# Optimization experiments

Measured on AMD Instinct MI355X. Metric: run time of the kernel, lower is better.

The kernel has to match this reference:

```python
import jax, jax.numpy as jnp
import numpy as np

MARGIN = 0.3
EPS = 1e-12


def setup_inputs() -> dict:
    key = jax.random.key(0)
    k1, k2 = jax.random.split(key)
    n, d = 4096, 1024
    inputs = jax.random.normal(k1, (n, d), dtype=jnp.float32)
    targets = jax.random.randint(k2, (n,), 0, 64, dtype=jnp.int64)
    return {"inputs": inputs, "targets": targets}


def reference(inputs, targets):
    n = inputs.shape[0]
    # pairwise Euclidean distance matrix: ||xi||^2 + ||xj||^2 - 2 xi.xj
    sq = jnp.sum(inputs * inputs, axis=1)  # [n]
    dist2 = sq[:, None] + sq[None, :] - 2.0 * (inputs @ inputs.T)
    dist = jnp.sqrt(jnp.clip(dist2, EPS))  # [n, n]
    # same-label mask (includes diagonal, matching original)
    mask = targets[:, None] == targets[None, :]
    # fused masked row-wise hard mining
    neg_inf = jnp.asarray(-jnp.inf, dist.dtype)
    pos_inf = jnp.asarray(jnp.inf, dist.dtype)
    dist_ap = jnp.max(jnp.where(mask, dist, neg_inf), axis=1)  # hardest positive
    dist_an = jnp.min(jnp.where(mask, pos_inf, dist), axis=1)  # hardest negative
    # MarginRankingLoss with y=1: mean(relu(margin - (dist_an - dist_ap)))
    loss = jnp.mean(jnp.maximum(MARGIN - (dist_an - dist_ap), 0.0))
    prec = jnp.sum((dist_an > dist_ap).astype(jnp.float32)) / n
    return (loss, prec)
```

## Files before the change

### kernel.cpp

```cpp
#include <hip/hip_runtime.h>
#include <stdint.h>

#define MARGIN 0.3f
#define EPS 1e-12f

typedef __attribute__((ext_vector_type(8))) __bf16 bf16x8;
typedef __attribute__((ext_vector_type(4))) float f32x4;

__device__ __forceinline__ unsigned short f2bf(float f) {
    unsigned u = __float_as_uint(f);
    unsigned r = (u + 0x7FFFu + ((u >> 16) & 1u)) >> 16;
    return (unsigned short)r;
}

#define GLD16(gp, lp)                                                     \
    __builtin_amdgcn_global_load_lds(                                     \
        (const __attribute__((address_space(1))) void*)(gp),              \
        (__attribute__((address_space(3))) void*)(lp), 16, 0, 0)

__global__ __launch_bounds__(256) void prep_kernel(
    const float* __restrict__ X, unsigned short* __restrict__ Xbf,
    float* __restrict__ sqg, unsigned* __restrict__ apb,
    unsigned* __restrict__ anb, unsigned* __restrict__ ctr, int d) {
    const int row = blockIdx.x;
    const int tid = threadIdx.x;
    const float4* Xr = (const float4*)(X + (size_t)row * d);
    float s = 0.0f;
    for (int idx = tid; idx < (d >> 2); idx += blockDim.x) {
        float4 v = Xr[idx];
        s += v.x * v.x + v.y * v.y + v.z * v.z + v.w * v.w;
        ushort4 o;
        o.x = f2bf(v.x); o.y = f2bf(v.y); o.z = f2bf(v.z); o.w = f2bf(v.w);
        ((ushort4*)(Xbf + (size_t)row * d))[idx] = o;
    }
    __shared__ float red[4];
    for (int off = 32; off > 0; off >>= 1) s += __shfl_down(s, off, 64);
    const int wave = tid >> 6, lane = tid & 63;
    if (lane == 0) red[wave] = s;
    __syncthreads();
    if (tid == 0) {
        sqg[row] = red[0] + red[1] + red[2] + red[3];
        apb[row] = 0u;
        anb[row] = 0x7F800000u;
        if (row == 0) ctr[0] = 0u;
    }
}

#define BM 128
#define BN 128
#define BK 32

__global__ __launch_bounds__(256) void tri_gemm(
    const unsigned short* __restrict__ Xbf, const float* __restrict__ sqg,
    const int* __restrict__ tgt, unsigned* __restrict__ apb,
    unsigned* __restrict__ anb, unsigned* __restrict__ ctr,
    float* __restrict__ out, int n, int d, int nblk) {
    __shared__ unsigned short ldsA[2][BM * BK];
    __shared__ unsigned short ldsB[2][BN * BK];

    const int tid  = threadIdx.x;
    const int lane = tid & 63;
    const int wave = tid >> 6;
    const int wm = wave >> 1, wn = wave & 1;
    const int lo = lane & 15, hi = lane >> 4;

    const int bid = blockIdx.x;
    int bi = (int)((sqrtf(8.0f * (float)bid + 1.0f) - 1.0f) * 0.5f);
    while ((bi + 1) * (bi + 2) / 2 <= bid) ++bi;
    while (bi * (bi + 1) / 2 > bid) --bi;
    const int bj = bid - bi * (bi + 1) / 2;
    const int rowBase = bi * BM;
    const int colBase = bj * BN;
    const bool offdiag = (bi != bj);

    const int lrow = lane >> 2;
    const int lk   = (lane & 3) * 8;

    f32x4 acc[4][4] = {};

    const int nt = d / BK;
    int cur = 0;
#pragma unroll
    for (int c2 = 0; c2 < 2; ++c2) {
        const int c = wave * 2 + c2;
        GLD16(Xbf + (size_t)(rowBase + c * 16 + lrow) * d + lk, &ldsA[0][c * 512]);
        GLD16(Xbf + (size_t)(colBase + c * 16 + lrow) * d + lk, &ldsB[0][c * 512]);
    }
    asm volatile("s_waitcnt vmcnt(0)" ::: "memory");
    __syncthreads();

    for (int t = 0; t < nt; ++t) {
        if (t + 1 < nt) {
            const int k0 = (t + 1) * BK;
#pragma unroll
            for (int c2 = 0; c2 < 2; ++c2) {
                const int c = wave * 2 + c2;
                GLD16(Xbf + (size_t)(rowBase + c * 16 + lrow) * d + k0 + lk,
                      &ldsA[cur ^ 1][c * 512]);
                GLD16(Xbf + (size_t)(colBase + c * 16 + lrow) * d + k0 + lk,
                      &ldsB[cur ^ 1][c * 512]);
            }
        }
        bf16x8 a[4], b[4];
#pragma unroll
        for (int mi = 0; mi < 4; ++mi)
            a[mi] = *(const bf16x8*)&ldsA[cur][(wm * 64 + mi * 16 + lo) * BK + hi * 8];
#pragma unroll
        for (int ni = 0; ni < 4; ++ni)
            b[ni] = *(const bf16x8*)&ldsB[cur][(wn * 64 + ni * 16 + lo) * BK + hi * 8];
#pragma unroll
        for (int mi = 0; mi < 4; ++mi)
#pragma unroll
            for (int ni = 0; ni < 4; ++ni)
                acc[mi][ni] = __builtin_amdgcn_mfma_f32_16x16x32_bf16(
                    a[mi], b[ni], acc[mi][ni], 0, 0, 0);
        if (t + 1 < nt) {
            asm volatile("s_waitcnt vmcnt(0)" ::: "memory");
            __syncthreads();
            cur ^= 1;
        }
    }

    float sqj[4];
    int   tj[4];
#pragma unroll
    for (int ni = 0; ni < 4; ++ni) {
        const int gj = colBase + wn * 64 + ni * 16 + lo;
        sqj[ni] = sqg[gj];
        tj[ni]  = tgt[gj];
    }
    float cap[4], can[4];
#pragma unroll
    for (int ni = 0; ni < 4; ++ni) { cap[ni] = 0.0f; can[ni] = __uint_as_float(0x7F800000u); }

#pragma unroll
    for (int mi = 0; mi < 4; ++mi) {
#pragma unroll
        for (int j = 0; j < 4; ++j) {
            const int gi = rowBase + wm * 64 + mi * 16 + hi * 4 + j;
            const float sqi = sqg[gi];
            const int   ti  = tgt[gi];
            float ap = 0.0f;
            float an = __uint_as_float(0x7F800000u);
#pragma unroll
            for (int ni = 0; ni < 4; ++ni) {
                const float d2 = sqi + sqj[ni] - 2.0f * acc[mi][ni][j];
                const float dist = sqrtf(fmaxf(d2, EPS));
                if (ti == tj[ni]) {
                    ap = fmaxf(ap, dist);
                    cap[ni] = fmaxf(cap[ni], dist);
                } else {
                    an = fminf(an, dist);
                    can[ni] = fminf(can[ni], dist);
                }
            }
#pragma unroll
            for (int m = 1; m < 16; m <<= 1) {
                ap = fmaxf(ap, __shfl_xor(ap, m, 64));
                an = fminf(an, __shfl_xor(an, m, 64));
            }
            if (lo == 0) {
                atomicMax(&apb[gi], __float_as_uint(ap));
                atomicMin(&anb[gi], __float_as_uint(an));
            }
        }
    }
    if (offdiag) {
#pragma unroll
        for (int ni = 0; ni < 4; ++ni) {
            float ap = cap[ni], an = can[ni];
#pragma unroll
            for (int m = 16; m < 64; m <<= 1) {
                ap = fmaxf(ap, __shfl_xor(ap, m, 64));
                an = fminf(an, __shfl_xor(an, m, 64));
            }
            if (hi == 0) {
                const int gj = colBase + wn * 64 + ni * 16 + lo;
                atomicMax(&apb[gj], __float_as_uint(ap));
                atomicMin(&anb[gj], __float_as_uint(an));
            }
        }
    }

    __threadfence();
    __syncthreads();
    __shared__ int lastFlag;
    if (tid == 0) {
        unsigned prev = __hip_atomic_fetch_add(ctr, 1u, __ATOMIC_ACQ_REL,
                                               __HIP_MEMORY_SCOPE_AGENT);
        lastFlag = (prev == (unsigned)(nblk - 1)) ? 1 : 0;
    }
    __syncthreads();
    if (lastFlag) {
        float ls = 0.0f, pc = 0.0f;
        for (int i = tid; i < n; i += 256) {
            const float ap = __uint_as_float(__hip_atomic_load(
                &apb[i], __ATOMIC_RELAXED, __HIP_MEMORY_SCOPE_AGENT));
            const float an = __uint_as_float(__hip_atomic_load(
                &anb[i], __ATOMIC_RELAXED, __HIP_MEMORY_SCOPE_AGENT));
            ls += fmaxf(MARGIN - (an - ap), 0.0f);
            pc += (an > ap) ? 1.0f : 0.0f;
        }
        __shared__ float rl[4], rp[4];
        for (int off = 32; off > 0; off >>= 1) {
            ls += __shfl_down(ls, off, 64);
            pc += __shfl_down(pc, off, 64);
        }
        if ((tid & 63) == 0) { rl[tid >> 6] = ls; rp[tid >> 6] = pc; }
        __syncthreads();
        if (tid == 0) {
            out[0] = (rl[0] + rl[1] + rl[2] + rl[3]) / (float)n;
            out[1] = (rp[0] + rp[1] + rp[2] + rp[3]) / (float)n;
        }
    }
}

__global__ __launch_bounds__(256) void fb_zero(float* __restrict__ out) {
    if (threadIdx.x == 0) { out[0] = 0.0f; out[1] = 0.0f; }
}

__global__ __launch_bounds__(256) void fb_row(
    const float* __restrict__ X, const int* __restrict__ tgt,
    float* __restrict__ out, int n, int d) {
    __shared__ float xi[4096];
    const int i = blockIdx.x;
    const int tid = threadIdx.x;
    for (int k = tid; k < d; k += 256) xi[k] = X[(size_t)i * d + k];
    __syncthreads();
    const int ti = tgt[i];
    float ap = 0.0f;
    float an = __uint_as_float(0x7F800000u);
    for (int j = tid; j < n; j += 256) {
        const float4* Xj = (const float4*)(X + (size_t)j * d);
        float s = 0.0f;
        for (int k4 = 0; k4 < (d >> 2); ++k4) {
            float4 v = Xj[k4];
            float4 u = *(const float4*)&xi[k4 * 4];
            float dx = u.x - v.x, dy = u.y - v.y, dz = u.z - v.z, dw = u.w - v.w;
            s += dx * dx + dy * dy + dz * dz + dw * dw;
        }
        const float dist = sqrtf(fmaxf(s, EPS));
        if (tgt[j] == ti) ap = fmaxf(ap, dist);
        else              an = fminf(an, dist);
    }
    for (int m = 1; m < 64; m <<= 1) {
        ap = fmaxf(ap, __shfl_xor(ap, m, 64));
        an = fminf(an, __shfl_xor(an, m, 64));
    }
    __shared__ float rap[4], ran[4];
    const int wave = tid >> 6, lane = tid & 63;
    if (lane == 0) { rap[wave] = ap; ran[wave] = an; }
    __syncthreads();
    if (tid == 0) {
        ap = fmaxf(fmaxf(rap[0], rap[1]), fmaxf(rap[2], rap[3]));
        an = fminf(fminf(ran[0], ran[1]), fminf(ran[2], ran[3]));
        atomicAdd(&out[0], fmaxf(MARGIN - (an - ap), 0.0f));
        atomicAdd(&out[1], (an > ap) ? 1.0f : 0.0f);
    }
}

__global__ __launch_bounds__(64) void fb_scale(float* __restrict__ out, float inv_n) {
    if (threadIdx.x == 0) { out[0] *= inv_n; out[1] *= inv_n; }
}

extern "C" void kernel_launch(void* const* d_in, const int* in_sizes, int n_in,
                              void* d_out, int out_size, void* d_ws, size_t ws_size,
                              hipStream_t stream) {
    const float* X   = (const float*)d_in[0];
    const int*   tgt = (const int*)d_in[1];
    const int n = in_sizes[1];
    const int d = in_sizes[0] / n;

    const size_t need = (size_t)n * d * 2 + (size_t)n * 4 * 3 + 4;
    if (ws_size >= need) {
        char* ws = (char*)d_ws;
        unsigned short* Xbf = (unsigned short*)ws;
        float*    sqg = (float*)(ws + (size_t)n * d * 2);
        unsigned* apb = (unsigned*)((char*)sqg + (size_t)n * 4);
        unsigned* anb = apb + n;
        unsigned* ctr = anb + n;

        const int nb = n / BM;
        const int nblk = nb * (nb + 1) / 2;
        prep_kernel<<<n, 256, 0, stream>>>(X, Xbf, sqg, apb, anb, ctr, d);
        tri_gemm<<<nblk, 256, 0, stream>>>(Xbf, sqg, tgt, apb, anb, ctr,
                                           (float*)d_out, n, d, nblk);
    } else {
        fb_zero<<<1, 256, 0, stream>>>((float*)d_out);
        fb_row<<<n, 256, 0, stream>>>(X, tgt, (float*)d_out, n, d);
        fb_scale<<<1, 64, 0, stream>>>((float*)d_out, 1.0f / (float)n);
    }
}
```

Baseline: 146.3 us.

## Load GEMM operands directly from global to registers, remap blocks per XCD

The triangular GEMM drops the LDS double-buffered global_load_lds staging. Each wave now loads its bf16 fragments straight from global memory into registers, ping-ponging two register sets across K steps with no barriers. Block IDs are remapped so consecutive tiles land on the same XCD for L2 locality, and the prep kernel now gives each wave one row. The cost is that tiles are no longer shared through LDS, so each wave re-reads from L2/global and global traffic grows, with uncoalesced 16-byte row-strided accesses.

After: 223.8 us. 1.53x slower.

```diff
diff --git a/kernel.cpp b/kernel.cpp
--- a/kernel.cpp
+++ b/kernel.cpp
@@ -13,37 +13,30 @@
     return (unsigned short)r;
 }
 
-#define GLD16(gp, lp)                                                     \
-    __builtin_amdgcn_global_load_lds(                                     \
-        (const __attribute__((address_space(1))) void*)(gp),              \
-        (__attribute__((address_space(3))) void*)(lp), 16, 0, 0)
-
 __global__ __launch_bounds__(256) void prep_kernel(
     const float* __restrict__ X, unsigned short* __restrict__ Xbf,
     float* __restrict__ sqg, unsigned* __restrict__ apb,
     unsigned* __restrict__ anb, unsigned* __restrict__ ctr, int d) {
-    const int row = blockIdx.x;
-    const int tid = threadIdx.x;
+    const int wave = threadIdx.x >> 6, lane = threadIdx.x & 63;
+    const int row = blockIdx.x * 4 + wave;
     const float4* Xr = (const float4*)(X + (size_t)row * d);
+    ushort4* Or = (ushort4*)(Xbf + (size_t)row * d);
     float s = 0.0f;
-    for (int idx = tid; idx < (d >> 2); idx += blockDim.x) {
-        float4 v = Xr[idx];
+    const int nq = d >> 2;
+    for (int i = lane; i < nq; i += 64) {
+        float4 v = Xr[i];
         s += v.x * v.x + v.y * v.y + v.z * v.z + v.w * v.w;
         ushort4 o;
         o.x = f2bf(v.x); o.y = f2bf(v.y); o.z = f2bf(v.z); o.w = f2bf(v.w);
-        ((ushort4*)(Xbf + (size_t)row * d))[idx] = o;
-    }
-    __shared__ float red[4];
+        Or[i] = o;
+    }
     for (int off = 32; off > 0; off >>= 1) s += __shfl_down(s, off, 64);
-    const int wave = tid >> 6, lane = tid & 63;
-    if (lane == 0) red[wave] = s;
-    __syncthreads();
-    if (tid == 0) {
-        sqg[row] = red[0] + red[1] + red[2] + red[3];
+    if (lane == 0) {
+        sqg[row] = s;
         apb[row] = 0u;
         anb[row] = 0x7F800000u;
-        if (row == 0) ctr[0] = 0u;
-    }
+    }
+    if (blockIdx.x == 0 && threadIdx.x == 0) ctr[0] = 0u;
 }
 
 #define BM 128
@@ -55,16 +48,17 @@
     const int* __restrict__ tgt, unsigned* __restrict__ apb,
     unsigned* __restrict__ anb, unsigned* __restrict__ ctr,
     float* __restrict__ out, int n, int d, int nblk) {
-    __shared__ unsigned short ldsA[2][BM * BK];
-    __shared__ unsigned short ldsB[2][BN * BK];
-
     const int tid  = threadIdx.x;
     const int lane = tid & 63;
     const int wave = tid >> 6;
     const int wm = wave >> 1, wn = wave & 1;
     const int lo = lane & 15, hi = lane >> 4;
 
-    const int bid = blockIdx.x;
+    const int orig = blockIdx.x;
+    const int q = nblk >> 3, r = nblk & 7;
+    const int xcd = orig & 7, idx = orig >> 3;
+    const int bid = (xcd < r ? xcd * (q + 1) : r * (q + 1) + (xcd - r) * q) + idx;
+
     int bi = (int)((sqrtf(8.0f * (float)bid + 1.0f) - 1.0f) * 0.5f);
     while ((bi + 1) * (bi + 2) / 2 <= bid) ++bi;
     while (bi * (bi + 1) / 2 > bid) --bi;
@@ -73,52 +67,49 @@
     const int colBase = bj * BN;
     const bool offdiag = (bi != bj);
 
-    const int lrow = lane >> 2;
-    const int lk   = (lane & 3) * 8;
+    const unsigned short* pA[4];
+    const unsigned short* pB[4];
+#pragma unroll
+    for (int mi = 0; mi < 4; ++mi)
+        pA[mi] = Xbf + (size_t)(rowBase + wm * 64 + mi * 16 + lo) * d + hi * 8;
+#pragma unroll
+    for (int ni = 0; ni < 4; ++ni)
+        pB[ni] = Xbf + (size_t)(colBase + wn * 64 + ni * 16 + lo) * d + hi * 8;
 
     f32x4 acc[4][4] = {};
-
-    const int nt = d / BK;
-    int cur = 0;
-#pragma unroll
-    for (int c2 = 0; c2 < 2; ++c2) {
-        const int c = wave * 2 + c2;
-        GLD16(Xbf + (size_t)(rowBase + c * 16 + lrow) * d + lk, &ldsA[0][c * 512]);
-        GLD16(Xbf + (size_t)(colBase + c * 16 + lrow) * d + lk, &ldsB[0][c * 512]);
-    }
-    asm volatile("s_waitcnt vmcnt(0)" ::: "memory");
-    __syncthreads();
-
-    for (int t = 0; t < nt; ++t) {
-        if (t + 1 < nt) {
-            const int k0 = (t + 1) * BK;
-#pragma unroll
-            for (int c2 = 0; c2 < 2; ++c2) {
-                const int c = wave * 2 + c2;
-                GLD16(Xbf + (size_t)(rowBase + c * 16 + lrow) * d + k0 + lk,
-                      &ldsA[cur ^ 1][c * 512]);
-                GLD16(Xbf + (size_t)(colBase + c * 16 + lrow) * d + k0 + lk,
-                      &ldsB[cur ^ 1][c * 512]);
-            }
-        }
-        bf16x8 a[4], b[4];
-#pragma unroll
-        for (int mi = 0; mi < 4; ++mi)
-            a[mi] = *(const bf16x8*)&ldsA[cur][(wm * 64 + mi * 16 + lo) * BK + hi * 8];
-#pragma unroll
-        for (int ni = 0; ni < 4; ++ni)
-            b[ni] = *(const bf16x8*)&ldsB[cur][(wn * 64 + ni * 16 + lo) * BK + hi * 8];
+    bf16x8 a0[4], b0[4], a1[4], b1[4];
+
+#pragma unroll
+    for (int i = 0; i < 4; ++i) {
+        a0[i] = *(const bf16x8*)(pA[i]);
+        b0[i] = *(const bf16x8*)(pB[i]);
+    }
+
+    for (int k0 = 0; k0 < d; k0 += 2 * BK) {
+        const int k1 = k0 + BK;
+        const int k2 = (k1 + BK < d) ? k1 + BK : 0;
+#pragma unroll
+        for (int i = 0; i < 4; ++i) {
+            a1[i] = *(const bf16x8*)(pA[i] + k1);
+            b1[i] = *(const bf16x8*)(pB[i] + k1);
+        }
 #pragma unroll
         for (int mi = 0; mi < 4; ++mi)
 #pragma unroll
             for (int ni = 0; ni < 4; ++ni)
                 acc[mi][ni] = __builtin_amdgcn_mfma_f32_16x16x32_bf16(
-                    a[mi], b[ni], acc[mi][ni], 0, 0, 0);
-        if (t + 1 < nt) {
-            asm volatile("s_waitcnt vmcnt(0)" ::: "memory");
-            __syncthreads();
-            cur ^= 1;
-        }
+                    a0[mi], b0[ni], acc[mi][ni], 0, 0, 0);
+#pragma unroll
+        for (int i = 0; i < 4; ++i) {
+            a0[i] = *(const bf16x8*)(pA[i] + k2);
+            b0[i] = *(const bf16x8*)(pB[i] + k2);
+        }
+#pragma unroll
+        for (int mi = 0; mi < 4; ++mi)
+#pragma unroll
+            for (int ni = 0; ni < 4; ++ni)
+                acc[mi][ni] = __builtin_amdgcn_mfma_f32_16x16x32_bf16(
+                    a1[mi], b1[ni], acc[mi][ni], 0, 0, 0);
     }
 
     float sqj[4];
@@ -282,7 +273,7 @@
 
         const int nb = n / BM;
         const int nblk = nb * (nb + 1) / 2;
-        prep_kernel<<<n, 256, 0, stream>>>(X, Xbf, sqg, apb, anb, ctr, d);
+        prep_kernel<<<n / 4, 256, 0, stream>>>(X, Xbf, sqg, apb, anb, ctr, d);
         tri_gemm<<<nblk, 256, 0, stream>>>(Xbf, sqg, tgt, apb, anb, ctr,
                                            (float*)d_out, n, d, nblk);
     } else {
```

## Use 8 waves per GEMM tile, XCD-aware block remap, and row-per-wave prep

Applied to the files above, without the earlier changes.

The triangular GEMM block grows from 4 to 8 waves, so each wave computes a 64x32 sub-tile with half the accumulators and issues one global-to-LDS load per matrix per k-step. Block IDs are remapped so consecutive triangular tiles land on the same XCD, which should improve L2 reuse of shared row and column panels. The prep kernel now gives each wave its own row, dropping the LDS reduction and block barrier. The trade-off is more per-block barrier traffic and duplicated A-fragment LDS reads across waves in exchange for higher occupancy and lower register pressure.

New measurement: 176.2 us. +20.4%, slower.

```diff
diff --git a/kernel.cpp b/kernel.cpp
--- a/kernel.cpp
+++ b/kernel.cpp
@@ -22,35 +22,33 @@
     const float* __restrict__ X, unsigned short* __restrict__ Xbf,
     float* __restrict__ sqg, unsigned* __restrict__ apb,
     unsigned* __restrict__ anb, unsigned* __restrict__ ctr, int d) {
-    const int row = blockIdx.x;
-    const int tid = threadIdx.x;
+    const int wave = threadIdx.x >> 6, lane = threadIdx.x & 63;
+    const int row = blockIdx.x * 4 + wave;
     const float4* Xr = (const float4*)(X + (size_t)row * d);
+    ushort4* Or = (ushort4*)(Xbf + (size_t)row * d);
     float s = 0.0f;
-    for (int idx = tid; idx < (d >> 2); idx += blockDim.x) {
-        float4 v = Xr[idx];
+    const int nq = d >> 2;
+    for (int i = lane; i < nq; i += 64) {
+        float4 v = Xr[i];
         s += v.x * v.x + v.y * v.y + v.z * v.z + v.w * v.w;
         ushort4 o;
         o.x = f2bf(v.x); o.y = f2bf(v.y); o.z = f2bf(v.z); o.w = f2bf(v.w);
-        ((ushort4*)(Xbf + (size_t)row * d))[idx] = o;
-    }
-    __shared__ float red[4];
+        Or[i] = o;
+    }
     for (int off = 32; off > 0; off >>= 1) s += __shfl_down(s, off, 64);
-    const int wave = tid >> 6, lane = tid & 63;
-    if (lane == 0) red[wave] = s;
-    __syncthreads();
-    if (tid == 0) {
-        sqg[row] = red[0] + red[1] + red[2] + red[3];
+    if (lane == 0) {
+        sqg[row] = s;
         apb[row] = 0u;
         anb[row] = 0x7F800000u;
-        if (row == 0) ctr[0] = 0u;
-    }
+    }
+    if (blockIdx.x == 0 && threadIdx.x == 0) ctr[0] = 0u;
 }
 
 #define BM 128
 #define BN 128
 #define BK 32
 
-__global__ __launch_bounds__(256) void tri_gemm(
+__global__ __launch_bounds__(512, 4) void tri_gemm(
     const unsigned short* __restrict__ Xbf, const float* __restrict__ sqg,
     const int* __restrict__ tgt, unsigned* __restrict__ apb,
     unsigned* __restrict__ anb, unsigned* __restrict__ ctr,
@@ -61,10 +59,15 @@
     const int tid  = threadIdx.x;
     const int lane = tid & 63;
     const int wave = tid >> 6;
-    const int wm = wave >> 1, wn = wave & 1;
+    const int wm = wave >> 2;
+    const int wn = wave & 3;
     const int lo = lane & 15, hi = lane >> 4;
 
-    const int bid = blockIdx.x;
+    const int orig = blockIdx.x;
+    const int q = nblk >> 3, r = nblk & 7;
+    const int xcd = orig & 7, idx = orig >> 3;
+    const int bid = (xcd < r ? xcd * (q + 1) : r * (q + 1) + (xcd - r) * q) + idx;
+
     int bi = (int)((sqrtf(8.0f * (float)bid + 1.0f) - 1.0f) * 0.5f);
     while ((bi + 1) * (bi + 2) / 2 <= bid) ++bi;
     while (bi * (bi + 1) / 2 > bid) --bi;
@@ -75,43 +78,35 @@
 
     const int lrow = lane >> 2;
     const int lk   = (lane & 3) * 8;
-
-    f32x4 acc[4][4] = {};
+    const unsigned short* gA0 = Xbf + (size_t)(rowBase + wave * 16 + lrow) * d + lk;
+    const unsigned short* gB0 = Xbf + (size_t)(colBase + wave * 16 + lrow) * d + lk;
+
+    f32x4 acc[4][2] = {};
 
     const int nt = d / BK;
     int cur = 0;
-#pragma unroll
-    for (int c2 = 0; c2 < 2; ++c2) {
-        const int c = wave * 2 + c2;
-        GLD16(Xbf + (size_t)(rowBase + c * 16 + lrow) * d + lk, &ldsA[0][c * 512]);
-        GLD16(Xbf + (size_t)(colBase + c * 16 + lrow) * d + lk, &ldsB[0][c * 512]);
-    }
+    GLD16(gA0, &ldsA[0][wave * 512]);
+    GLD16(gB0, &ldsB[0][wave * 512]);
     asm volatile("s_waitcnt vmcnt(0)" ::: "memory");
     __syncthreads();
 
     for (int t = 0; t < nt; ++t) {
         if (t + 1 < nt) {
             const int k0 = (t + 1) * BK;
-#pragma unroll
-            for (int c2 = 0; c2 < 2; ++c2) {
-                const int c = wave * 2 + c2;
-                GLD16(Xbf + (size_t)(rowBase + c * 16 + lrow) * d + k0 + lk,
-                      &ldsA[cur ^ 1][c * 512]);
-                GLD16(Xbf + (size_t)(colBase + c * 16 + lrow) * d + k0 + lk,
-                      &ldsB[cur ^ 1][c * 512]);
-            }
-        }
-        bf16x8 a[4], b[4];
+            GLD16(gA0 + k0, &ldsA[cur ^ 1][wave * 512]);
+            GLD16(gB0 + k0, &ldsB[cur ^ 1][wave * 512]);
+        }
+        bf16x8 a[4], b[2];
 #pragma unroll
         for (int mi = 0; mi < 4; ++mi)
             a[mi] = *(const bf16x8*)&ldsA[cur][(wm * 64 + mi * 16 + lo) * BK + hi * 8];
 #pragma unroll
-        for (int ni = 0; ni < 4; ++ni)
-            b[ni] = *(const bf16x8*)&ldsB[cur][(wn * 64 + ni * 16 + lo) * BK + hi * 8];
+        for (int ni = 0; ni < 2; ++ni)
+            b[ni] = *(const bf16x8*)&ldsB[cur][(wn * 32 + ni * 16 + lo) * BK + hi * 8];
 #pragma unroll
         for (int mi = 0; mi < 4; ++mi)
 #pragma unroll
-            for (int ni = 0; ni < 4; ++ni)
+            for (int ni = 0; ni < 2; ++ni)
                 acc[mi][ni] = __builtin_amdgcn_mfma_f32_16x16x32_bf16(
                     a[mi], b[ni], acc[mi][ni], 0, 0, 0);
         if (t + 1 < nt) {
@@ -121,17 +116,17 @@
         }
     }
 
-    float sqj[4];
-    int   tj[4];
-#pragma unroll
-    for (int ni = 0; ni < 4; ++ni) {
-        const int gj = colBase + wn * 64 + ni * 16 + lo;
+    float sqj[2];
+    int   tj[2];
+#pragma unroll
+    for (int ni = 0; ni < 2; ++ni) {
+        const int gj = colBase + wn * 32 + ni * 16 + lo;
         sqj[ni] = sqg[gj];
         tj[ni]  = tgt[gj];
     }
-    float cap[4], can[4];
-#pragma unroll
-    for (int ni = 0; ni < 4; ++ni) { cap[ni] = 0.0f; can[ni] = __uint_as_float(0x7F800000u); }
+    float cap[2], can[2];
+#pragma unroll
+    for (int ni = 0; ni < 2; ++ni) { cap[ni] = 0.0f; can[ni] = __uint_as_float(0x7F800000u); }
 
 #pragma unroll
     for (int mi = 0; mi < 4; ++mi) {
@@ -143,7 +138,7 @@
             float ap = 0.0f;
             float an = __uint_as_float(0x7F800000u);
 #pragma unroll
-            for (int ni = 0; ni < 4; ++ni) {
+            for (int ni = 0; ni < 2; ++ni) {
                 const float d2 = sqi + sqj[ni] - 2.0f * acc[mi][ni][j];
                 const float dist = sqrtf(fmaxf(d2, EPS));
                 if (ti == tj[ni]) {
@@ -167,7 +162,7 @@
     }
     if (offdiag) {
 #pragma unroll
-        for (int ni = 0; ni < 4; ++ni) {
+        for (int ni = 0; ni < 2; ++ni) {
             float ap = cap[ni], an = can[ni];
 #pragma unroll
             for (int m = 16; m < 64; m <<= 1) {
@@ -175,7 +170,7 @@
                 an = fminf(an, __shfl_xor(an, m, 64));
             }
             if (hi == 0) {
-                const int gj = colBase + wn * 64 + ni * 16 + lo;
+                const int gj = colBase + wn * 32 + ni * 16 + lo;
                 atomicMax(&apb[gj], __float_as_uint(ap));
                 atomicMin(&anb[gj], __float_as_uint(an));
             }
@@ -193,7 +188,7 @@
     __syncthreads();
     if (lastFlag) {
         float ls = 0.0f, pc = 0.0f;
-        for (int i = tid; i < n; i += 256) {
+        for (int i = tid; i < n; i += 512) {
             const float ap = __uint_as_float(__hip_atomic_load(
                 &apb[i], __ATOMIC_RELAXED, __HIP_MEMORY_SCOPE_AGENT));
             const float an = __uint_as_float(__hip_atomic_load(
@@ -201,7 +196,7 @@
             ls += fmaxf(MARGIN - (an - ap), 0.0f);
             pc += (an > ap) ? 1.0f : 0.0f;
         }
-        __shared__ float rl[4], rp[4];
+        __shared__ float rl[8], rp[8];
         for (int off = 32; off > 0; off >>= 1) {
             ls += __shfl_down(ls, off, 64);
             pc += __shfl_down(pc, off, 64);
@@ -209,8 +204,11 @@
         if ((tid & 63) == 0) { rl[tid >> 6] = ls; rp[tid >> 6] = pc; }
         __syncthreads();
         if (tid == 0) {
-            out[0] = (rl[0] + rl[1] + rl[2] + rl[3]) / (float)n;
-            out[1] = (rp[0] + rp[1] + rp[2] + rp[3]) / (float)n;
+            float L = 0.0f, P = 0.0f;
+#pragma unroll
+            for (int w = 0; w < 8; ++w) { L += rl[w]; P += rp[w]; }
+            out[0] = L / (float)n;
+            out[1] = P / (float)n;
         }
     }
 }
@@ -282,8 +280,8 @@
 
         const int nb = n / BM;
         const int nblk = nb * (nb + 1) / 2;
-        prep_kernel<<<n, 256, 0, stream>>>(X, Xbf, sqg, apb, anb, ctr, d);
-        tri_gemm<<<nblk, 256, 0, stream>>>(Xbf, sqg, tgt, apb, anb, ctr,
+        prep_kernel<<<n / 4, 256, 0, stream>>>(X, Xbf, sqg, apb, anb, ctr, d);
+        tri_gemm<<<nblk, 512, 0, stream>>>(Xbf, sqg, tgt, apb, anb, ctr,
                                            (float*)d_out, n, d, nblk);
     } else {
         fb_zero<<<1, 256, 0, stream>>>((float*)d_out);
```
